# Performance work log

Measured on AMD Instinct MI355X. Metric: run time of the kernel, lower is better.

## Reference

```python
import jax, jax.numpy as jnp
import numpy as np

N_TOKENS = 16384
DIM = 7168
N_EXPERTS = 256
N_GROUPS = 8
TOPK_GROUPS = 4
TOPK = 8
ROUTE_SCALE = 2.5


def setup_inputs() -> dict:
    key = jax.random.key(0)
    k1, k2 = jax.random.split(key)
    x = jax.random.normal(k1, (N_TOKENS, DIM), dtype=jnp.float32)
    # kaiming_uniform_(a=sqrt(5)) -> Uniform(-1/sqrt(fan_in), 1/sqrt(fan_in))
    bound = 1.0 / np.sqrt(DIM)
    weight = jax.random.uniform(k2, (N_EXPERTS, DIM), dtype=jnp.float32,
                                minval=-bound, maxval=bound)
    expert_bias = jnp.zeros((N_EXPERTS,), dtype=jnp.float32)
    return {"x": x, "weight": weight, "expert_bias": expert_bias}


def reference(x, weight, expert_bias):
    n = x.shape[0]
    # linear scoring + sigmoid (score_func == 'sigmoid')
    scores = jax.nn.sigmoid(x @ weight.T)            # [n, E]
    biased = scores + expert_bias                    # [n, E]
    # group-limited routing
    bg = biased.reshape(n, N_GROUPS, -1)             # [n, G, E/G]
    top2, _ = jax.lax.top_k(bg, 2)
    group_scores = top2.sum(axis=-1)                 # [n, G]
    _, top_group_idx = jax.lax.top_k(group_scores, TOPK_GROUPS)  # [n, TOPK_GROUPS]
    keep = jax.nn.one_hot(top_group_idx, N_GROUPS, dtype=jnp.float32).sum(axis=1) > 0  # [n, G]
    masked = jnp.where(keep[:, :, None], bg, -jnp.inf).reshape(n, -1)  # [n, E]
    # final top-k over allowed experts
    _, indices = jax.lax.top_k(masked, TOPK)         # [n, TOPK]
    weights = jnp.take_along_axis(scores, indices, axis=1)
    weights = weights / (weights.sum(axis=-1, keepdims=True) + 1e-20)
    weights = weights * ROUTE_SCALE
    return weights.astype(x.dtype), indices
```

## Files before the change

kernel.cpp:

```cpp
#include <hip/hip_runtime.h>
#include <math.h>

#define MTOK 16384
#define NEXP 256
#define KDIM 7168

#define CAPR 1024
#define KSPLIT 8
#define KCH (KDIM / KSPLIT)
#define TAU 2e-5f

#define NKC 224
#define NSTEP 112

typedef _Float16 f16;
typedef __attribute__((ext_vector_type(8))) f16 f16x8;
typedef __attribute__((ext_vector_type(4))) f16 f16x4;
typedef __attribute__((ext_vector_type(4))) float f32x4;

__device__ __forceinline__ void cvt_hilo(const float4 a, const float4 b, f16x8* h, f16x8* l) {
    float xs[8] = {a.x, a.y, a.z, a.w, b.x, b.y, b.z, b.w};
#pragma unroll
    for (int e = 0; e < 8; ++e) {
        f16 hh = (f16)xs[e];
        (*h)[e] = hh;
        (*l)[e] = (f16)((xs[e] - (float)hh) * 2048.f);
    }
}

__device__ __forceinline__ void cvt_hilo4(const float4 a, f16x4* h, f16x4* l) {
    float xs[4] = {a.x, a.y, a.z, a.w};
#pragma unroll
    for (int e = 0; e < 4; ++e) {
        f16 hh = (f16)xs[e];
        (*h)[e] = hh;
        (*l)[e] = (f16)((xs[e] - (float)hh) * 2048.f);
    }
}

__global__ void wconv_k(const float* __restrict__ W, f16* __restrict__ Wfrag) {
    const int e  = blockIdx.x;
    const int kc = threadIdx.x;
    if (kc >= NKC) return;
    const int nt  = e >> 4;
    const int col = e & 15;
    const float* src = W + (size_t)e * KDIM + kc * 32;
    float x[32];
#pragma unroll
    for (int i = 0; i < 8; ++i) {
        float4 v = *(const float4*)(src + i * 4);
        x[i * 4 + 0] = v.x; x[i * 4 + 1] = v.y; x[i * 4 + 2] = v.z; x[i * 4 + 3] = v.w;
    }
#pragma unroll
    for (int k8 = 0; k8 < 4; ++k8) {
        f16x8 h, l;
#pragma unroll
        for (int j = 0; j < 8; ++j) {
            float xv = x[k8 * 8 + j];
            f16 hh = (f16)xv;
            h[j] = hh;
            l[j] = (f16)((xv - (float)hh) * 2048.f);
        }
        const size_t lanepos = (size_t)(k8 * 16 + col) * 8;
        *(f16x8*)(Wfrag + (((size_t)(0 * 16 + nt) * NKC + kc) << 9) + lanepos) = h;
        *(f16x8*)(Wfrag + (((size_t)(1 * 16 + nt) * NKC + kc) << 9) + lanepos) = l;
    }
}

__launch_bounds__(512, 2)
__global__ void gemm_v10_k(const float* __restrict__ X,
                           const f16* __restrict__ Wfrag,
                           float* __restrict__ S) {
    __shared__ f16 A_lds[2][2][8][128][8];

    const int tid  = threadIdx.x;
    const int lane = tid & 63;
    const int w    = tid >> 6;
    const int wr   = w >> 2;
    const int wc   = w & 3;

    const int id   = blockIdx.x;
    const int xcd  = id & 7;
    const int nb   = xcd >> 2;
    const int mb   = (id >> 3) * 4 + (xcd & 3);
    const int m0 = mb * 128;
    const int n0 = nb * 128;

    const int arow = tid >> 2;
    const int kl   = tid & 3;
    const float* xg = X + (size_t)(m0 + arow) * KDIM + kl * 4;
    const int ghalf = (kl & 1) * 4;
    const int gbase = kl >> 1;

    const int fr = lane & 15;
    const int fq = lane >> 4;

    const int ntb = nb * 8 + wc * 2;
    const f16* wpH0 = Wfrag + (((size_t)(ntb + 0)  * NKC) << 9) + lane * 8;
    const f16* wpH1 = Wfrag + (((size_t)(ntb + 1)  * NKC) << 9) + lane * 8;
    const f16* wpL0 = Wfrag + (((size_t)(ntb + 16) * NKC) << 9) + lane * 8;
    const f16* wpL1 = Wfrag + (((size_t)(ntb + 17) * NKC) << 9) + lane * 8;

    f32x4 accA[4][2];
    f32x4 accB[4][2];
#pragma unroll
    for (int i = 0; i < 4; ++i)
#pragma unroll
        for (int j = 0; j < 2; ++j) { accA[i][j] = (f32x4)0.f; accB[i][j] = (f32x4)0.f; }

    float4 aE0, aE1, aE2, aE3, aO0, aO1, aO2, aO3;
    f16x8 p0, p1, p2, p3, p4, p5, p6, p7;
    f16x8 q0, q1, q2, q3, q4, q5, q6, q7;

#define A_LOAD4(R0_, R1_, R2_, R3_, STEP_) do {                             \
        const int st_ = (STEP_) < NSTEP ? (STEP_) : (NSTEP - 1);            \
        const float* p_ = xg + (size_t)st_ * 64;                            \
        R0_ = *(const float4*)(p_ + 0);                                     \
        R1_ = *(const float4*)(p_ + 16);                                    \
        R2_ = *(const float4*)(p_ + 32);                                    \
        R3_ = *(const float4*)(p_ + 48);                                    \
    } while (0)

#define B_LOAD8(R0_,R1_,R2_,R3_,R4_,R5_,R6_,R7_, STEP_) do {                \
        const int st_ = (STEP_) < NSTEP ? (STEP_) : (NSTEP - 1);            \
        const size_t oa_ = ((size_t)(st_ * 2))     << 9;                    \
        const size_t ob_ = ((size_t)(st_ * 2 + 1)) << 9;                    \
        R0_ = *(const f16x8*)(wpH0 + oa_);                                  \
        R1_ = *(const f16x8*)(wpH1 + oa_);                                  \
        R2_ = *(const f16x8*)(wpL0 + oa_);                                  \
        R3_ = *(const f16x8*)(wpL1 + oa_);                                  \
        R4_ = *(const f16x8*)(wpH0 + ob_);                                  \
        R5_ = *(const f16x8*)(wpH1 + ob_);                                  \
        R6_ = *(const f16x8*)(wpL0 + ob_);                                  \
        R7_ = *(const f16x8*)(wpL1 + ob_);                                  \
    } while (0)

#define ST_HG(BUF_, R_, I_) do {                                            \
        f16x4 h_, l_;                                                       \
        cvt_hilo4(R_, &h_, &l_);                                            \
        *(f16x4*)&A_lds[BUF_][0][gbase + 2 * (I_)][arow][ghalf] = h_;       \
        *(f16x4*)&A_lds[BUF_][1][gbase + 2 * (I_)][arow][ghalf] = l_;       \
    } while (0)

#define STORE_A4(BUF_, R0_, R1_, R2_, R3_) do {                             \
        ST_HG(BUF_, R0_, 0);                                                \
        ST_HG(BUF_, R1_, 1);                                                \
        ST_HG(BUF_, R2_, 2);                                                \
        ST_HG(BUF_, R3_, 3);                                                \
    } while (0)

#define MFMA16(A_, B_, C_) __builtin_amdgcn_mfma_f32_16x16x32_f16(A_, B_, C_, 0, 0, 0)

#define COMPUTE_CH(BUF_, K8O_, H0_, H1_, L0_, L1_) do {                     \
        f16x8 ah_[4], al_[4];                                               \
        _Pragma("unroll")                                                   \
        for (int mi_ = 0; mi_ < 4; ++mi_) {                                 \
            const int r_ = wr * 64 + mi_ * 16 + fr;                         \
            ah_[mi_] = *(const f16x8*)&A_lds[BUF_][0][(K8O_) + fq][r_][0];  \
            al_[mi_] = *(const f16x8*)&A_lds[BUF_][1][(K8O_) + fq][r_][0];  \
        }                                                                   \
        _Pragma("unroll")                                                   \
        for (int mi_ = 0; mi_ < 4; ++mi_) {                                 \
            accA[mi_][0] = MFMA16(ah_[mi_], H0_, accA[mi_][0]);             \
            accA[mi_][1] = MFMA16(ah_[mi_], H1_, accA[mi_][1]);             \
            accB[mi_][0] = MFMA16(ah_[mi_], L0_, accB[mi_][0]);             \
            accB[mi_][0] = MFMA16(al_[mi_], H0_, accB[mi_][0]);             \
            accB[mi_][1] = MFMA16(ah_[mi_], L1_, accB[mi_][1]);             \
            accB[mi_][1] = MFMA16(al_[mi_], H1_, accB[mi_][1]);             \
        }                                                                   \
    } while (0)

    A_LOAD4(aE0, aE1, aE2, aE3, 0);
    A_LOAD4(aO0, aO1, aO2, aO3, 1);
    B_LOAD8(p0, p1, p2, p3, p4, p5, p6, p7, 0);
    STORE_A4(0, aE0, aE1, aE2, aE3);
    __syncthreads();

    for (int s = 0; s < NSTEP; s += 2) {
        A_LOAD4(aE0, aE1, aE2, aE3, s + 2);
        B_LOAD8(q0, q1, q2, q3, q4, q5, q6, q7, s + 1);
        COMPUTE_CH(0, 0, p0, p1, p2, p3);
        COMPUTE_CH(0, 4, p4, p5, p6, p7);
        STORE_A4(1, aO0, aO1, aO2, aO3);
        __syncthreads();

        A_LOAD4(aO0, aO1, aO2, aO3, s + 3);
        B_LOAD8(p0, p1, p2, p3, p4, p5, p6, p7, s + 2);
        COMPUTE_CH(1, 0, q0, q1, q2, q3);
        COMPUTE_CH(1, 4, q4, q5, q6, q7);
        STORE_A4(0, aE0, aE1, aE2, aE3);
        __syncthreads();
    }

#pragma unroll
    for (int mi = 0; mi < 4; ++mi)
#pragma unroll
        for (int ni = 0; ni < 2; ++ni) {
            const int e = n0 + wc * 32 + ni * 16 + fr;
#pragma unroll
            for (int r = 0; r < 4; ++r) {
                const int m = m0 + wr * 64 + mi * 16 + fq * 4 + r;
                float logit = accA[mi][ni][r] + accB[mi][ni][r] * (1.f / 2048.f);
                S[(size_t)m * NEXP + e] = 1.f / (1.f + expf(-logit));
            }
        }
#undef A_LOAD4
#undef B_LOAD8
#undef ST_HG
#undef STORE_A4
#undef MFMA16
#undef COMPUTE_CH
}

__launch_bounds__(256)
__global__ void route_flag_k(const float* __restrict__ S,
                             const float* __restrict__ bias,
                             float* __restrict__ out,
                             int* __restrict__ list,
                             int* __restrict__ count) {
    __shared__ float sraw[4][256];
    const int wv   = threadIdx.x >> 6;
    const int lane = threadIdx.x & 63;
    const int token = blockIdx.x * 4 + wv;
    const float NINF = -__builtin_inff();
    const float PINF =  __builtin_inff();

    const float* row = S + (size_t)token * NEXP;
    float4 v = *(const float4*)(row + lane * 4);
    *(float4*)&sraw[wv][lane * 4] = v;

    const int e0 = lane * 4;
    float4 bi4 = *(const float4*)(bias + e0);
    float b0 = v.x + bi4.x;
    float b1 = v.y + bi4.y;
    float b2 = v.z + bi4.z;
    float b3 = v.w + bi4.w;

    bool flag = false;

    float m1 = b0, m2 = NINF;
    if (b1 > m1) { m2 = m1; m1 = b1; } else if (b1 > m2) m2 = b1;
    if (b2 > m1) { m2 = m1; m1 = b2; } else if (b2 > m2) m2 = b2;
    if (b3 > m1) { m2 = m1; m1 = b3; } else if (b3 > m2) m2 = b3;
#pragma unroll
    for (int w = 1; w <= 4; w <<= 1) {
        float o1 = __shfl_xor(m1, w);
        float o2 = __shfl_xor(m2, w);
        float nm1 = fmaxf(m1, o1);
        float nm2 = fmaxf(fminf(m1, o1), fmaxf(m2, o2));
        m1 = nm1; m2 = nm2;
    }
    const float gs = m1 + m2;
    const int g = lane >> 3;

    int rank = 0;
#pragma unroll
    for (int j = 0; j < 8; ++j) {
        float gj = __shfl(gs, j * 8);
        rank += (gj > gs) || (gj == gs && j < g);
    }
    const bool sel = rank < 4;

    {
        float a = sel ? gs : PINF;
        float b = sel ? NINF : gs;
#pragma unroll
        for (int w = 1; w < 64; w <<= 1) {
            a = fminf(a, __shfl_xor(a, w));
            b = fmaxf(b, __shfl_xor(b, w));
        }
        flag |= (a - b) < 2.f * TAU;
    }

    if (!sel) { b0 = NINF; b1 = NINF; b2 = NINF; b3 = NINF; }

    int myidx = 0;
    float prev = 0.f;
#pragma unroll
    for (int it = 0; it < 9; ++it) {
        float bv = b0; int bi = e0;
        if (b1 > bv) { bv = b1; bi = e0 + 1; }
        if (b2 > bv) { bv = b2; bi = e0 + 2; }
        if (b3 > bv) { bv = b3; bi = e0 + 3; }
#pragma unroll
        for (int w = 1; w < 64; w <<= 1) {
            float ov = __shfl_xor(bv, w);
            int   oi = __shfl_xor(bi, w);
            if (ov > bv || (ov == bv && oi < bi)) { bv = ov; bi = oi; }
        }
        if (it > 0) flag |= (prev - bv) < TAU;
        prev = bv;
        if (it < 8) {
            if (lane == it) myidx = bi;
            if ((bi >> 2) == lane) {
                switch (bi & 3) {
                    case 0: b0 = NINF; break;
                    case 1: b1 = NINF; break;
                    case 2: b2 = NINF; break;
                    case 3: b3 = NINF; break;
                }
            }
        }
    }

    const bool anyflag = __any((int)flag);

    __syncthreads();

    float wval = (lane < 8) ? sraw[wv][myidx] : 0.f;
    float s = wval;
    s += __shfl_xor(s, 1);
    s += __shfl_xor(s, 2);
    s += __shfl_xor(s, 4);
    if (lane < 8) {
        float wout = wval / (s + 1e-20f) * 2.5f;
        out[(size_t)token * 8 + lane] = wout;
        out[(size_t)MTOK * 8 + (size_t)token * 8 + lane] = (float)myidx;
    }

    if (anyflag && lane == 0) {
        int f = atomicAdd(count, 1);
        if (f < CAPR) list[f] = token;
    }
}

__launch_bounds__(256)
__global__ void rescore_k(const float* __restrict__ X,
                          const float* __restrict__ W,
                          const int* __restrict__ list,
                          const int* __restrict__ count,
                          double* __restrict__ Ldp) {
    const int cnt = min(*count, CAPR);
    const int m0 = blockIdx.x * 64;
    if (m0 >= cnt) return;
    const int n0 = blockIdx.y * 64;
    const int ks = blockIdx.z;
    const int kbase = ks * KCH;

    __shared__ float As[16][66];
    __shared__ float Bs[16][66];
    const int tid = threadIdx.x;
    const int row = tid >> 2;
    const int c   = tid & 3;
    const int tm  = tid >> 4;
    const int tn  = tid & 15;

    const int gi = list[min(m0 + row, cnt - 1)];
    const float* xg = X + (size_t)gi * KDIM + c * 4;
    const float* wg = W + (size_t)(n0 + row) * KDIM + c * 4;

    double acc[4][4];
#pragma unroll
    for (int i = 0; i < 4; ++i)
#pragma unroll
        for (int j = 0; j < 4; ++j) acc[i][j] = 0.0;

    for (int k0 = kbase; k0 < kbase + KCH; k0 += 16) {
        float4 a = *(const float4*)(xg + k0);
        float4 b = *(const float4*)(wg + k0);
        __syncthreads();
        As[c * 4 + 0][row] = a.x; As[c * 4 + 1][row] = a.y;
        As[c * 4 + 2][row] = a.z; As[c * 4 + 3][row] = a.w;
        Bs[c * 4 + 0][row] = b.x; Bs[c * 4 + 1][row] = b.y;
        Bs[c * 4 + 2][row] = b.z; Bs[c * 4 + 3][row] = b.w;
        __syncthreads();
#pragma unroll
        for (int k = 0; k < 16; ++k) {
            double ad[4], bd[4];
#pragma unroll
            for (int i = 0; i < 4; ++i) ad[i] = (double)As[k][tm * 4 + i];
#pragma unroll
            for (int j = 0; j < 4; ++j) bd[j] = (double)Bs[k][tn * 4 + j];
#pragma unroll
            for (int i = 0; i < 4; ++i)
#pragma unroll
                for (int j = 0; j < 4; ++j)
                    acc[i][j] = fma(ad[i], bd[j], acc[i][j]);
        }
    }

#pragma unroll
    for (int i = 0; i < 4; ++i) {
        const int r = m0 + tm * 4 + i;
        if (r < cnt) {
#pragma unroll
            for (int j = 0; j < 4; ++j)
                Ldp[((size_t)ks * CAPR + r) * NEXP + n0 + tn * 4 + j] = acc[i][j];
        }
    }
}

__launch_bounds__(64)
__global__ void route_exact_k(const double* __restrict__ Ldp,
                              const float* __restrict__ bias,
                              const int* __restrict__ list,
                              const int* __restrict__ count,
                              float* __restrict__ out) {
    const int cnt = min(*count, CAPR);
    const int f = blockIdx.x;
    if (f >= cnt) return;
    const int lane = threadIdx.x;
    const int token = list[f];
    const double NINF = -__builtin_inf();

    const int e0 = lane * 4;
    double l0 = 0.0, l1 = 0.0, l2 = 0.0, l3 = 0.0;
#pragma unroll
    for (int s = 0; s < KSPLIT; ++s) {
        double4 p = *(const double4*)(Ldp + ((size_t)s * CAPR + f) * NEXP + e0);
        l0 += p.x; l1 += p.y; l2 += p.z; l3 += p.w;
    }

    double s0 = 1.0 / (1.0 + exp(-l0));
    double s1 = 1.0 / (1.0 + exp(-l1));
    double s2 = 1.0 / (1.0 + exp(-l2));
    double s3 = 1.0 / (1.0 + exp(-l3));

    float4 bi4 = *(const float4*)(bias + e0);
    double b0 = s0 + (double)bi4.x;
    double b1 = s1 + (double)bi4.y;
    double b2 = s2 + (double)bi4.z;
    double b3 = s3 + (double)bi4.w;

    double m1 = b0, m2 = NINF;
    if (b1 > m1) { m2 = m1; m1 = b1; } else if (b1 > m2) m2 = b1;
    if (b2 > m1) { m2 = m1; m1 = b2; } else if (b2 > m2) m2 = b2;
    if (b3 > m1) { m2 = m1; m1 = b3; } else if (b3 > m2) m2 = b3;
#pragma unroll
    for (int w = 1; w <= 4; w <<= 1) {
        double o1 = __shfl_xor(m1, w);
        double o2 = __shfl_xor(m2, w);
        double nm1 = fmax(m1, o1);
        double nm2 = fmax(fmin(m1, o1), fmax(m2, o2));
        m1 = nm1; m2 = nm2;
    }
    const double gs = m1 + m2;
    const int g = lane >> 3;

    int rank = 0;
#pragma unroll
    for (int j = 0; j < 8; ++j) {
        double gj = __shfl(gs, j * 8);
        rank += (gj > gs) || (gj == gs && j < g);
    }
    if (rank >= 4) { b0 = NINF; b1 = NINF; b2 = NINF; b3 = NINF; }

    int myidx = 0;
#pragma unroll
    for (int it = 0; it < 8; ++it) {
        double bv = b0; int bi = e0;
        if (b1 > bv) { bv = b1; bi = e0 + 1; }
        if (b2 > bv) { bv = b2; bi = e0 + 2; }
        if (b3 > bv) { bv = b3; bi = e0 + 3; }
#pragma unroll
        for (int w = 1; w < 64; w <<= 1) {
            double ov = __shfl_xor(bv, w);
            int    oi = __shfl_xor(bi, w);
            if (ov > bv || (ov == bv && oi < bi)) { bv = ov; bi = oi; }
        }
        if (lane == it) myidx = bi;
        if ((bi >> 2) == lane) {
            switch (bi & 3) {
                case 0: b0 = NINF; break;
                case 1: b1 = NINF; break;
                case 2: b2 = NINF; break;
                case 3: b3 = NINF; break;
            }
        }
    }

    double g0 = __shfl(s0, myidx >> 2);
    double g1 = __shfl(s1, myidx >> 2);
    double g2 = __shfl(s2, myidx >> 2);
    double g3 = __shfl(s3, myidx >> 2);
    const int ss = myidx & 3;
    double wval = (lane < 8) ? (ss == 0 ? g0 : ss == 1 ? g1 : ss == 2 ? g2 : g3) : 0.0;
    double s = wval;
    s += __shfl_xor(s, 1);
    s += __shfl_xor(s, 2);
    s += __shfl_xor(s, 4);
    if (lane < 8) {
        float wout = (float)(wval / (s + 1e-20) * 2.5);
        out[(size_t)token * 8 + lane] = wout;
        out[(size_t)MTOK * 8 + (size_t)token * 8 + lane] = (float)myidx;
    }
}

__global__ void init_k(int* count) { *count = 0; }

extern "C" void kernel_launch(void* const* d_in, const int* in_sizes, int n_in,
                              void* d_out, int out_size, void* d_ws, size_t ws_size,
                              hipStream_t stream) {
    const float* X    = (const float*)d_in[0];
    const float* W    = (const float*)d_in[1];
    const float* bias = (const float*)d_in[2];
    float* out = (float*)d_out;

    float*  Lf    = (float*)d_ws;
    double* Ldp   = (double*)d_ws;
    int*    list  = (int*)((char*)d_ws + 16777216);
    int*    cnt   = (int*)((char*)d_ws + 16777216 + CAPR * 4);
    f16*    Wfrag = (f16*)((char*)d_ws + 16777216 + 65536);

    init_k<<<1, 1, 0, stream>>>(cnt);
    wconv_k<<<NEXP, 256, 0, stream>>>(W, Wfrag);

    gemm_v10_k<<<256, 512, 0, stream>>>(X, Wfrag, Lf);

    route_flag_k<<<MTOK / 4, 256, 0, stream>>>(Lf, bias, out, list, cnt);

    dim3 g3(CAPR / 64, NEXP / 64, KSPLIT);
    rescore_k<<<g3, 256, 0, stream>>>(X, W, list, cnt, Ldp);

    route_exact_k<<<CAPR, 64, 0, stream>>>(Ldp, bias, list, cnt, out);
}
```

Baseline: 386.0 us.

## Split GEMM into 128x64 tiles over 512 blocks and fold counter init into wconv

The scoring GEMM now uses 128-row by 64-expert tiles with a 4x2 wave grid, each wave holding 32x32 outputs. This doubles the grid to 512 blocks and raises the occupancy hint to 4 blocks per CU, so the 256 CUs get more concurrent work instead of one wave of 256 blocks. The cost is that each A tile is now loaded and converted to hi/lo fp16 twice, once per extra N tile, which doubles X reads and conversion work. The separate init kernel is also removed by zeroing the counter inside wconv_k, saving one launch.

```diff
diff --git a/kernel.cpp b/kernel.cpp
--- a/kernel.cpp
+++ b/kernel.cpp
@@ -18,16 +18,6 @@
 typedef __attribute__((ext_vector_type(4))) f16 f16x4;
 typedef __attribute__((ext_vector_type(4))) float f32x4;
 
-__device__ __forceinline__ void cvt_hilo(const float4 a, const float4 b, f16x8* h, f16x8* l) {
-    float xs[8] = {a.x, a.y, a.z, a.w, b.x, b.y, b.z, b.w};
-#pragma unroll
-    for (int e = 0; e < 8; ++e) {
-        f16 hh = (f16)xs[e];
-        (*h)[e] = hh;
-        (*l)[e] = (f16)((xs[e] - (float)hh) * 2048.f);
-    }
-}
-
 __device__ __forceinline__ void cvt_hilo4(const float4 a, f16x4* h, f16x4* l) {
     float xs[4] = {a.x, a.y, a.z, a.w};
 #pragma unroll
@@ -38,7 +28,9 @@
     }
 }
 
-__global__ void wconv_k(const float* __restrict__ W, f16* __restrict__ Wfrag) {
+__global__ void wconv_k(const float* __restrict__ W, f16* __restrict__ Wfrag,
+                        int* __restrict__ count) {
+    if (blockIdx.x == 0 && threadIdx.x == 0) *count = 0;
     const int e  = blockIdx.x;
     const int kc = threadIdx.x;
     if (kc >= NKC) return;
@@ -67,8 +59,8 @@
     }
 }
 
-__launch_bounds__(512, 2)
-__global__ void gemm_v10_k(const float* __restrict__ X,
+__launch_bounds__(512, 4)
+__global__ void gemm_v11_k(const float* __restrict__ X,
                            const f16* __restrict__ Wfrag,
                            float* __restrict__ S) {
     __shared__ f16 A_lds[2][2][8][128][8];
@@ -76,15 +68,15 @@
     const int tid  = threadIdx.x;
     const int lane = tid & 63;
     const int w    = tid >> 6;
-    const int wr   = w >> 2;
-    const int wc   = w & 3;
+    const int wm   = w >> 1;
+    const int wn   = w & 1;
 
     const int id   = blockIdx.x;
     const int xcd  = id & 7;
-    const int nb   = xcd >> 2;
-    const int mb   = (id >> 3) * 4 + (xcd & 3);
+    const int nq   = xcd & 3;
+    const int mb   = (id >> 3) * 2 + (xcd >> 2);
     const int m0 = mb * 128;
-    const int n0 = nb * 128;
+    const int n0 = nq * 64;
 
     const int arow = tid >> 2;
     const int kl   = tid & 3;
@@ -95,16 +87,16 @@
     const int fr = lane & 15;
     const int fq = lane >> 4;
 
-    const int ntb = nb * 8 + wc * 2;
+    const int ntb = nq * 4 + wn * 2;
     const f16* wpH0 = Wfrag + (((size_t)(ntb + 0)  * NKC) << 9) + lane * 8;
     const f16* wpH1 = Wfrag + (((size_t)(ntb + 1)  * NKC) << 9) + lane * 8;
     const f16* wpL0 = Wfrag + (((size_t)(ntb + 16) * NKC) << 9) + lane * 8;
     const f16* wpL1 = Wfrag + (((size_t)(ntb + 17) * NKC) << 9) + lane * 8;
 
-    f32x4 accA[4][2];
-    f32x4 accB[4][2];
-#pragma unroll
-    for (int i = 0; i < 4; ++i)
+    f32x4 accA[2][2];
+    f32x4 accB[2][2];
+#pragma unroll
+    for (int i = 0; i < 2; ++i)
 #pragma unroll
         for (int j = 0; j < 2; ++j) { accA[i][j] = (f32x4)0.f; accB[i][j] = (f32x4)0.f; }
 
@@ -152,15 +144,15 @@
 #define MFMA16(A_, B_, C_) __builtin_amdgcn_mfma_f32_16x16x32_f16(A_, B_, C_, 0, 0, 0)
 
 #define COMPUTE_CH(BUF_, K8O_, H0_, H1_, L0_, L1_) do {                     \
-        f16x8 ah_[4], al_[4];                                               \
+        f16x8 ah_[2], al_[2];                                               \
         _Pragma("unroll")                                                   \
-        for (int mi_ = 0; mi_ < 4; ++mi_) {                                 \
-            const int r_ = wr * 64 + mi_ * 16 + fr;                         \
+        for (int mi_ = 0; mi_ < 2; ++mi_) {                                 \
+            const int r_ = wm * 32 + mi_ * 16 + fr;                         \
             ah_[mi_] = *(const f16x8*)&A_lds[BUF_][0][(K8O_) + fq][r_][0];  \
             al_[mi_] = *(const f16x8*)&A_lds[BUF_][1][(K8O_) + fq][r_][0];  \
         }                                                                   \
         _Pragma("unroll")                                                   \
-        for (int mi_ = 0; mi_ < 4; ++mi_) {                                 \
+        for (int mi_ = 0; mi_ < 2; ++mi_) {                                 \
             accA[mi_][0] = MFMA16(ah_[mi_], H0_, accA[mi_][0]);             \
             accA[mi_][1] = MFMA16(ah_[mi_], H1_, accA[mi_][1]);             \
             accB[mi_][0] = MFMA16(ah_[mi_], L0_, accB[mi_][0]);             \
@@ -193,13 +185,13 @@
     }
 
 #pragma unroll
-    for (int mi = 0; mi < 4; ++mi)
+    for (int mi = 0; mi < 2; ++mi)
 #pragma unroll
         for (int ni = 0; ni < 2; ++ni) {
-            const int e = n0 + wc * 32 + ni * 16 + fr;
+            const int e = n0 + wn * 32 + ni * 16 + fr;
 #pragma unroll
             for (int r = 0; r < 4; ++r) {
-                const int m = m0 + wr * 64 + mi * 16 + fq * 4 + r;
+                const int m = m0 + wm * 32 + mi * 16 + fq * 4 + r;
                 float logit = accA[mi][ni][r] + accB[mi][ni][r] * (1.f / 2048.f);
                 S[(size_t)m * NEXP + e] = 1.f / (1.f + expf(-logit));
             }
@@ -486,8 +478,6 @@
     }
 }
 
-__global__ void init_k(int* count) { *count = 0; }
-
 extern "C" void kernel_launch(void* const* d_in, const int* in_sizes, int n_in,
                               void* d_out, int out_size, void* d_ws, size_t ws_size,
                               hipStream_t stream) {
@@ -502,10 +492,9 @@
     int*    cnt   = (int*)((char*)d_ws + 16777216 + CAPR * 4);
     f16*    Wfrag = (f16*)((char*)d_ws + 16777216 + 65536);
 
-    init_k<<<1, 1, 0, stream>>>(cnt);
-    wconv_k<<<NEXP, 256, 0, stream>>>(W, Wfrag);
-
-    gemm_v10_k<<<256, 512, 0, stream>>>(X, Wfrag, Lf);
+    wconv_k<<<NEXP, 256, 0, stream>>>(W, Wfrag, cnt);
+
+    gemm_v11_k<<<512, 512, 0, stream>>>(X, Wfrag, Lf);
 
     route_flag_k<<<MTOK / 4, 256, 0, stream>>>(Lf, bias, out, list, cnt);
 
```

Result: slower. 510.9 us (+32.4%).
